# Optimization experiments

Hardware: AMD Instinct MI355X
Metric: run time of the kernel (lower is better)

The kernel has to match this reference:

```python
import jax, jax.numpy as jnp
import numpy as np

B, C, H, W = 32, 256, 64, 64
EPS = 1e-8  # clamp for cosine-similarity denominators


def setup_inputs() -> dict:
    key = jax.random.key(0)
    k1, k2, k3 = jax.random.split(key, 3)
    unmasked = jax.random.normal(k1, (B, C, H, W), dtype=jnp.float32)
    masked = jax.random.normal(k2, (B, C, H, W), dtype=jnp.float32)
    latent_mask = jax.random.randint(k3, (B, H, W), 0, 2, dtype=jnp.int32)
    return {
        "unmasked_latent_tensors": unmasked,
        "masked_latent_tensors": masked,
        "latent_mask": latent_mask,
    }


def reference(unmasked_latent_tensors, masked_latent_tensors, latent_mask):
    # Original torch code builds a full [B, B*H*W, H, W] cross-activation of a
    # cosine-similarity 1x1 conv (input vs. every masked position used as a
    # prototype), then gathers only the diagonal entries where batch index and
    # spatial position match. Mathematically that diagonal is just the
    # per-position cosine similarity along the channel axis, computed here
    # directly.
    u = unmasked_latent_tensors
    m = masked_latent_tensors
    num = jnp.sum(u * m, axis=1)                       # [B, H, W]
    u_norm = jnp.sqrt(jnp.sum(u * u, axis=1))          # [B, H, W]
    m_norm = jnp.sqrt(jnp.sum(m * m, axis=1))          # [B, H, W]
    sim = num / (jnp.maximum(u_norm, EPS) * jnp.maximum(m_norm, EPS))
    # masked=True: average similarity over mask==1 positions.
    mask_f = (latent_mask != 0).astype(sim.dtype)      # [B, H, W]
    return jnp.sum(sim * mask_f) / jnp.sum(mask_f)
```

## Files before the change

### kernel.cpp

```cpp
#include <hip/hip_runtime.h>


#define BB   32
#define CC   256
#define HWSZ 4096
#define NPOS (BB * HWSZ)
#define HW4  (HWSZ / 4)
#define PPB  256
#define NW   8
#define CPW  (CC / NW)
#define NBLK (NPOS / PPB)
#define HALFBLK (NBLK / 2)
#define SIM_EPS 1e-8f

typedef float f32x4 __attribute__((ext_vector_type(4)));

template<bool NT>
__global__ __launch_bounds__(512) void
sim_half_kernel(const f32x4* __restrict__ u4,
                const f32x4* __restrict__ m4,
                const int*   __restrict__ mask,
                double*      __restrict__ ws,
                float*       __restrict__ out,
                int pos_base)
{
    __shared__ f32x4 s_num[NW][64];
    __shared__ f32x4 s_uu [NW][64];
    __shared__ f32x4 s_mm [NW][64];

    const int wv = threadIdx.x >> 6;
    const int l  = threadIdx.x & 63;

    const int pos0 = pos_base + blockIdx.x * PPB;
    const int b    = pos0 >> 12;
    const int hw0  = pos0 & (HWSZ - 1);

    int mk = 0;
    if (threadIdx.x < PPB) mk = mask[pos0 + threadIdx.x];

    const size_t base4 = (size_t)b * CC * HW4
                       + (size_t)(wv * CPW) * HW4
                       + (size_t)(hw0 >> 2) + (size_t)l;
    const f32x4* __restrict__ up = u4 + base4;
    const f32x4* __restrict__ mp = m4 + base4;

    f32x4 num = {0.f, 0.f, 0.f, 0.f};
    f32x4 uu  = {0.f, 0.f, 0.f, 0.f};
    f32x4 mm  = {0.f, 0.f, 0.f, 0.f};

#pragma unroll 4
    for (int c = 0; c < CPW; ++c) {
        f32x4 a, bv;
        if constexpr (NT) {
            a  = __builtin_nontemporal_load(up + (size_t)c * HW4);
            bv = __builtin_nontemporal_load(mp + (size_t)c * HW4);
        } else {
            a  = up[(size_t)c * HW4];
            bv = mp[(size_t)c * HW4];
        }
        num[0] = fmaf(a[0], bv[0], num[0]);
        num[1] = fmaf(a[1], bv[1], num[1]);
        num[2] = fmaf(a[2], bv[2], num[2]);
        num[3] = fmaf(a[3], bv[3], num[3]);
        uu[0]  = fmaf(a[0], a[0],  uu[0]);
        uu[1]  = fmaf(a[1], a[1],  uu[1]);
        uu[2]  = fmaf(a[2], a[2],  uu[2]);
        uu[3]  = fmaf(a[3], a[3],  uu[3]);
        mm[0]  = fmaf(bv[0], bv[0], mm[0]);
        mm[1]  = fmaf(bv[1], bv[1], mm[1]);
        mm[2]  = fmaf(bv[2], bv[2], mm[2]);
        mm[3]  = fmaf(bv[3], bv[3], mm[3]);
    }

    s_num[wv][l] = num;
    s_uu [wv][l] = uu;
    s_mm [wv][l] = mm;
    __syncthreads();

    double sd = 0.0, md = 0.0;
    if (threadIdx.x < PPB) {
        const int t = threadIdx.x;
        float fn = 0.f, fu = 0.f, fm = 0.f;
#pragma unroll
        for (int k = 0; k < NW; ++k) {
            fn += ((const float*)s_num[k])[t];
            fu += ((const float*)s_uu [k])[t];
            fm += ((const float*)s_mm [k])[t];
        }
        const float denom = fmaxf(sqrtf(fu), SIM_EPS) * fmaxf(sqrtf(fm), SIM_EPS);
        const float sim   = fn / denom;
        if (mk != 0) { sd = (double)sim; md = 1.0; }
    }

#pragma unroll
    for (int off = 32; off > 0; off >>= 1) {
        sd += __shfl_down(sd, off, 64);
        md += __shfl_down(md, off, 64);
    }

    __shared__ double r_s[NW];
    __shared__ double r_m[NW];
    if (l == 0) { r_s[wv] = sd; r_m[wv] = md; }
    __syncthreads();

    if (threadIdx.x == 0) {
        double ts = 0.0, tm = 0.0;
#pragma unroll
        for (int k = 0; k < NW; ++k) { ts += r_s[k]; tm += r_m[k]; }
        atomicAdd(&ws[0], ts);
        atomicAdd(&ws[1], tm);
        __threadfence();
        const unsigned long long prev =
            atomicAdd((unsigned long long*)&ws[2], 1ull);
        if (prev == (unsigned long long)(NBLK - 1)) {
            const double s  = atomicAdd(&ws[0], 0.0);
            const double mc = atomicAdd(&ws[1], 0.0);
            out[0] = (float)(s / mc);
        }
    }
}

extern "C" void kernel_launch(void* const* d_in, const int* in_sizes, int n_in,
                              void* d_out, int out_size, void* d_ws, size_t ws_size,
                              hipStream_t stream)
{
    const f32x4* u4   = (const f32x4*)d_in[0];
    const f32x4* m4   = (const f32x4*)d_in[1];
    const int*   mask = (const int*)d_in[2];
    float*  out = (float*)d_out;
    double* ws  = (double*)d_ws;

    hipMemsetAsync(d_ws, 0, 3 * sizeof(double), stream);

    sim_half_kernel<true ><<<HALFBLK, 512, 0, stream>>>(u4, m4, mask, ws, out, 0);
    sim_half_kernel<false><<<HALFBLK, 512, 0, stream>>>(u4, m4, mask, ws, out,
                                                        HALFBLK * PPB);
}
```

Before: 285.0 us.

## Stream channel tiles through LDS via global_load_lds double buffering

```diff
diff --git a/kernel.cpp b/kernel.cpp
--- a/kernel.cpp
+++ b/kernel.cpp
@@ -8,56 +8,63 @@
 #define HW4  (HWSZ / 4)
 #define PPB  256
 #define NW   8
-#define CPW  (CC / NW)
 #define NBLK (NPOS / PPB)
-#define HALFBLK (NBLK / 2)
+#define NSTEP (CC / NW)
 #define SIM_EPS 1e-8f
 
 typedef float f32x4 __attribute__((ext_vector_type(4)));
 
-template<bool NT>
+__device__ __forceinline__ void dma16(const f32x4* g, f32x4* lds)
+{
+    __builtin_amdgcn_global_load_lds(
+        (const __attribute__((address_space(1))) void*)g,
+        (__attribute__((address_space(3))) void*)lds,
+        16, 0, 0);
+}
+
 __global__ __launch_bounds__(512) void
-sim_half_kernel(const f32x4* __restrict__ u4,
-                const f32x4* __restrict__ m4,
-                const int*   __restrict__ mask,
-                double*      __restrict__ ws,
-                float*       __restrict__ out,
-                int pos_base)
+sim_dma_kernel(const f32x4* __restrict__ u4,
+               const f32x4* __restrict__ m4,
+               const int*   __restrict__ mask,
+               double*      __restrict__ ws,
+               float*       __restrict__ out)
 {
+    __shared__ f32x4 lds_u[2][NW][64];
+    __shared__ f32x4 lds_m[2][NW][64];
     __shared__ f32x4 s_num[NW][64];
     __shared__ f32x4 s_uu [NW][64];
     __shared__ f32x4 s_mm [NW][64];
 
-    const int wv = threadIdx.x >> 6;
-    const int l  = threadIdx.x & 63;
+    const int w = threadIdx.x >> 6;
+    const int l = threadIdx.x & 63;
 
-    const int pos0 = pos_base + blockIdx.x * PPB;
-    const int b    = pos0 >> 12;
-    const int hw0  = pos0 & (HWSZ - 1);
+    const int pos0  = blockIdx.x * PPB;
+    const int b     = pos0 >> 12;
+    const int hw4_0 = (pos0 & (HWSZ - 1)) >> 2;
 
     int mk = 0;
     if (threadIdx.x < PPB) mk = mask[pos0 + threadIdx.x];
 
-    const size_t base4 = (size_t)b * CC * HW4
-                       + (size_t)(wv * CPW) * HW4
-                       + (size_t)(hw0 >> 2) + (size_t)l;
-    const f32x4* __restrict__ up = u4 + base4;
-    const f32x4* __restrict__ mp = m4 + base4;
+    const size_t lane_base = (size_t)b * CC * HW4 + (size_t)hw4_0 + (size_t)l;
+
+    dma16(u4 + lane_base + (size_t)w * HW4, &lds_u[0][w][0]);
+    dma16(m4 + lane_base + (size_t)w * HW4, &lds_m[0][w][0]);
+    __syncthreads();
 
     f32x4 num = {0.f, 0.f, 0.f, 0.f};
     f32x4 uu  = {0.f, 0.f, 0.f, 0.f};
     f32x4 mm  = {0.f, 0.f, 0.f, 0.f};
 
-#pragma unroll 4
-    for (int c = 0; c < CPW; ++c) {
-        f32x4 a, bv;
-        if constexpr (NT) {
-            a  = __builtin_nontemporal_load(up + (size_t)c * HW4);
-            bv = __builtin_nontemporal_load(mp + (size_t)c * HW4);
-        } else {
-            a  = up[(size_t)c * HW4];
-            bv = mp[(size_t)c * HW4];
+#pragma unroll 2
+    for (int s = 0; s < NSTEP; ++s) {
+        const int cur = s & 1;
+        if (s + 1 < NSTEP) {
+            const size_t c = (size_t)((s + 1) * NW + w);
+            dma16(u4 + lane_base + c * HW4, &lds_u[cur ^ 1][w][0]);
+            dma16(m4 + lane_base + c * HW4, &lds_m[cur ^ 1][w][0]);
         }
+        const f32x4 a  = lds_u[cur][w][l];
+        const f32x4 bv = lds_m[cur][w][l];
         num[0] = fmaf(a[0], bv[0], num[0]);
         num[1] = fmaf(a[1], bv[1], num[1]);
         num[2] = fmaf(a[2], bv[2], num[2]);
@@ -70,11 +77,12 @@
         mm[1]  = fmaf(bv[1], bv[1], mm[1]);
         mm[2]  = fmaf(bv[2], bv[2], mm[2]);
         mm[3]  = fmaf(bv[3], bv[3], mm[3]);
+        __syncthreads();
     }
 
-    s_num[wv][l] = num;
-    s_uu [wv][l] = uu;
-    s_mm [wv][l] = mm;
+    s_num[w][l] = num;
+    s_uu [w][l] = uu;
+    s_mm [w][l] = mm;
     __syncthreads();
 
     double sd = 0.0, md = 0.0;
@@ -100,7 +108,7 @@
 
     __shared__ double r_s[NW];
     __shared__ double r_m[NW];
-    if (l == 0) { r_s[wv] = sd; r_m[wv] = md; }
+    if (l == 0) { r_s[w] = sd; r_m[w] = md; }
     __syncthreads();
 
     if (threadIdx.x == 0) {
@@ -132,7 +140,5 @@
 
     hipMemsetAsync(d_ws, 0, 3 * sizeof(double), stream);
 
-    sim_half_kernel<true ><<<HALFBLK, 512, 0, stream>>>(u4, m4, mask, ws, out, 0);
-    sim_half_kernel<false><<<HALFBLK, 512, 0, stream>>>(u4, m4, mask, ws, out,
-                                                        HALFBLK * PPB);
+    sim_dma_kernel<<<NBLK, 512, 0, stream>>>(u4, m4, mask, ws, out);
 }
```

Result: slower. 293.1 us (+2.8%).
